# Performance work log

Hardware: AMD Instinct MI355X
Metric: run time of the kernel (lower is better)

The kernel has to match this reference:

```python
import jax, jax.numpy as jnp
import numpy as np

B = 8; C = 128; EXP = 4; H = 112; W = 112; K = 3; PAD = 1; STRIDE = 1
IN_C = C * EXP  # 512
EPS = 1e-5


def setup_inputs() -> dict:
    key = jax.random.key(0)
    ks = jax.random.split(key, 24)
    f32 = jnp.float32

    def n(k, shape, s=0.05):
        return jax.random.normal(k, shape, f32) * s

    def bn_params(k):
        k1, k2, k3, k4 = jax.random.split(k, 4)
        g = 1.0 + 0.1 * jax.random.normal(k1, (), f32)  # placeholder, per-channel below
        return k1, k2, k3, k4

    inp = {}
    inp["x"] = jax.random.normal(ks[0], (B, IN_C, H, W), f32)
    # conv1: 1x1, 512 -> 128
    inp["w1"] = n(ks[1], (C, IN_C))
    inp["b1"] = n(ks[2], (C,))
    # bn1
    inp["g1"] = 1.0 + 0.1 * jax.random.normal(ks[3], (C,), f32)
    inp["be1"] = 0.1 * jax.random.normal(ks[4], (C,), f32)
    inp["m1"] = 0.1 * jax.random.normal(ks[5], (C,), f32)
    inp["v1"] = 1.0 + 0.1 * jax.random.uniform(ks[6], (C,), f32)
    # offset conv: 3x3, C -> 18 (small weights so sampling offsets stay modest)
    inp["woff"] = n(ks[7], (2 * K * K, C, K, K), 0.01)
    inp["boff"] = jnp.zeros((2 * K * K,), f32)
    # deformable conv weight: 3x3, C -> C
    inp["wd"] = n(ks[8], (C, C, K, K))
    inp["bd"] = n(ks[9], (C,))
    # bn2
    inp["g2"] = 1.0 + 0.1 * jax.random.normal(ks[10], (C,), f32)
    inp["be2"] = 0.1 * jax.random.normal(ks[11], (C,), f32)
    inp["m2"] = 0.1 * jax.random.normal(ks[12], (C,), f32)
    inp["v2"] = 1.0 + 0.1 * jax.random.uniform(ks[13], (C,), f32)
    # conv2: 1x1, 128 -> 512
    inp["w2"] = n(ks[14], (IN_C, C))
    inp["b2"] = n(ks[15], (IN_C,))
    # bn3
    inp["g3"] = 1.0 + 0.1 * jax.random.normal(ks[16], (IN_C,), f32)
    inp["be3"] = 0.1 * jax.random.normal(ks[17], (IN_C,), f32)
    inp["m3"] = 0.1 * jax.random.normal(ks[18], (IN_C,), f32)
    inp["v3"] = 1.0 + 0.1 * jax.random.uniform(ks[19], (IN_C,), f32)
    return inp


def conv1x1(x, w, b):
    return jnp.einsum("oc,bchw->bohw", w, x) + b[None, :, None, None]


def bn(x, g, be, m, v):
    inv = g / jnp.sqrt(v + EPS)
    return x * inv[None, :, None, None] + (be - m * inv)[None, :, None, None]


def conv3x3(x, w, b):
    out = jax.lax.conv_general_dilated(
        x, w, (STRIDE, STRIDE), ((PAD, PAD), (PAD, PAD)),
        dimension_numbers=("NCHW", "OIHW", "NCHW"))
    return out + b[None, :, None, None]


def deform_conv(x, offset, w, b):
    # x: [B, Cin, H, W]; offset: [B, 2*K*K, Ho, Wo] (y,x interleaved per kernel pt)
    Bn, Cin, Hh, Ww = x.shape
    Ho, Wo = offset.shape[2], offset.shape[3]
    P = Ho * Wo
    off = offset.reshape(Bn, K * K, 2, Ho, Wo)
    kk = jnp.arange(K * K)
    ky = (kk // K).astype(jnp.float32)  # 0..2
    kx = (kk % K).astype(jnp.float32)
    base_y = jnp.arange(Ho, dtype=jnp.float32) * STRIDE - PAD
    base_x = jnp.arange(Wo, dtype=jnp.float32) * STRIDE - PAD
    py = base_y[None, None, :, None] + ky[None, :, None, None] + off[:, :, 0]  # [B,9,Ho,Wo]
    px = base_x[None, None, None, :] + kx[None, :, None, None] + off[:, :, 1]
    y0 = jnp.floor(py); x0 = jnp.floor(px)
    dy = (py - y0).reshape(Bn, 1, -1)  # [B,1,9*P]
    dx = (px - x0).reshape(Bn, 1, -1)
    x_flat = x.reshape(Bn, Cin, Hh * Ww)

    def gather(yi, xi):
        valid = ((yi >= 0) & (yi <= Hh - 1) & (xi >= 0) & (xi <= Ww - 1))
        yc = jnp.clip(yi, 0, Hh - 1).astype(jnp.int32)
        xc = jnp.clip(xi, 0, Ww - 1).astype(jnp.int32)
        idx = (yc * Ww + xc).reshape(Bn, -1)  # [B, 9*P]
        g = jax.vmap(lambda xb, ib: xb[:, ib])(x_flat, idx)  # [B, Cin, 9*P]
        return g * valid.reshape(Bn, 1, -1).astype(x.dtype)

    v00 = gather(y0, x0)
    v01 = gather(y0, x0 + 1)
    v10 = gather(y0 + 1, x0)
    v11 = gather(y0 + 1, x0 + 1)
    cols = (v00 * (1 - dy) * (1 - dx) + v01 * (1 - dy) * dx
            + v10 * dy * (1 - dx) + v11 * dy * dx)  # [B, Cin, 9*P]
    cols = cols.reshape(Bn, Cin * K * K, P)
    out = jnp.einsum("oi,bip->bop", w.reshape(w.shape[0], -1), cols)
    out = out + b[None, :, None]
    return out.reshape(Bn, w.shape[0], Ho, Wo)


def reference(x, w1, b1, g1, be1, m1, v1, woff, boff, wd, bd,
              g2, be2, m2, v2, w2, b2, g3, be3, m3, v3):
    out = jax.nn.relu(bn(conv1x1(x, w1, b1), g1, be1, m1, v1))
    offset = conv3x3(out, woff, boff)
    out = deform_conv(out, offset, wd, bd)
    out = bn(out, g2, be2, m2, v2)
    out = bn(conv1x1(out, w2, b2), g3, be3, m3, v3)
    return jax.nn.relu(out + x)
```

## Files before the change

### kernel.cpp

```cpp
#include <hip/hip_runtime.h>
#include <hip/hip_bf16.h>


typedef __attribute__((ext_vector_type(8))) short short8;
typedef __attribute__((ext_vector_type(4))) float f32x4;

constexpr int Bn = 8;
constexpr int IC = 512;
constexpr int Cc = 128;
constexpr int Hh = 112;
constexpr int Ww = 112;
constexpr int Pp = Hh * Ww;
constexpr float EPSf = 1e-5f;

constexpr size_t OFS_OFFS  = 0;
constexpr size_t OFS_OUT2B = 2097152;
constexpr size_t OFS_W1B   = (size_t)Bn * Pp * IC / 2;
constexpr size_t OFS_W2B   = OFS_W1B + (size_t)Cc * IC / 2;
constexpr size_t OFS_WDB   = OFS_W2B + (size_t)IC * Cc / 2;
constexpr size_t OFS_WOFB  = OFS_WDB + (size_t)9 * Cc * Cc / 2;

__device__ __forceinline__ ushort f2bf(float f) {
  uint u = __float_as_uint(f);
  return (ushort)((u + 0x7fffu + ((u >> 16) & 1u)) >> 16);
}
__device__ __forceinline__ float bfLO(uint u) {
  return __uint_as_float(u << 16);
}
__device__ __forceinline__ float bfHI(uint u) {
  return __uint_as_float(u & 0xffff0000u);
}
__device__ __forceinline__ uint cvtpk(float a, float b) {
  __hip_bfloat162 h = __float22bfloat162_rn(make_float2(a, b));
  return *(uint*)&h;
}

__global__ __launch_bounds__(256) void prep_kernel(
    const float* __restrict__ w1, const float* __restrict__ w2,
    const float* __restrict__ wd, const float* __restrict__ woff,
    float* __restrict__ ws) {
  ushort* w1b  = (ushort*)(ws + OFS_W1B);
  ushort* w2b  = (ushort*)(ws + OFS_W2B);
  ushort* wdb  = (ushort*)(ws + OFS_WDB);
  ushort* wofb = (ushort*)(ws + OFS_WOFB);
  const int n1 = Cc * IC;
  const int n2 = IC * Cc;
  const int n3 = 9 * Cc * Cc;
  const int n4 = 9 * 32 * Cc;
  const int total = n1 + n2 + n3 + n4;
  for (int idx = blockIdx.x * blockDim.x + threadIdx.x; idx < total;
       idx += gridDim.x * blockDim.x) {
    if (idx < n1) {
      w1b[idx] = f2bf(w1[idx]);
    } else if (idx < n1 + n2) {
      int t = idx - n1;
      w2b[t] = f2bf(w2[t]);
    } else if (idx < n1 + n2 + n3) {
      int t = idx - n1 - n2;
      int k = t / (Cc * Cc), r = t % (Cc * Cc);
      int oc = r / Cc, ic = r % Cc;
      wdb[t] = f2bf(wd[(oc * Cc + ic) * 9 + k]);
    } else {
      int t = idx - n1 - n2 - n3;
      int k = t / (32 * Cc), r = t % (32 * Cc);
      int oc = r / Cc, ic = r % Cc;
      wofb[t] = (oc < 18) ? f2bf(woff[(oc * Cc + ic) * 9 + k]) : (ushort)0;
    }
  }
}

__global__ __launch_bounds__(256) void k1_fused_mfma(
    const float* __restrict__ x, const ushort* __restrict__ w1b,
    const float* __restrict__ b1, const float* __restrict__ g1,
    const float* __restrict__ be1, const float* __restrict__ m1,
    const float* __restrict__ v1, ushort* __restrict__ out1b) {
  __shared__ ushort smem[26624];

  const int tid = threadIdx.x;
  const int lane = tid & 63;
  const int wv = tid >> 6;
  const int lr = lane & 15, lg = lane >> 4;
  const int orig = blockIdx.x;
  const int bid = (orig & 7) * 98 + (orig >> 3);
  const int bi = bid / 98;
  const int pblk = (bid % 98) * 128;

  float xs[2][4][2][2];
  short8 wsv[2][2];

#define BAR_LGKM asm volatile("s_waitcnt lgkmcnt(0)\ns_barrier" ::: "memory")

#define LOADX(c, s)                                                       \
  {                                                                       \
    const float* xb_ = x + ((size_t)bi * IC + (size_t)((c) * 32 + wv * 8)) * Pp \
                         + pblk + lane;                                   \
    _Pragma("unroll") for (int q = 0; q < 4; ++q) {                       \
      _Pragma("unroll") for (int p = 0; p < 2; ++p) {                     \
        xs[s][q][p][0] = xb_[(size_t)(2 * q + p) * Pp];                   \
        xs[s][q][p][1] = xb_[(size_t)(2 * q + p) * Pp + 64];              \
      }                                                                   \
    }                                                                     \
  }

#define LOADW(c, s)                                                       \
  {                                                                       \
    const ushort* wb_ = w1b + (size_t)(wv * 32 + (lane >> 2)) * IC        \
                            + (c) * 32 + (lane & 3) * 8;                  \
    wsv[s][0] = *(const short8*)(wb_);                                    \
    wsv[s][1] = *(const short8*)(wb_ + (size_t)16 * IC);                  \
  }

#define WRITE(c, s)                                                       \
  {                                                                       \
    char* atb_ = (char*)smem + ((c) & 1) * 16384;                         \
    _Pragma("unroll") for (int e = 0; e < 2; ++e) {                       \
      const int px_ = lane + 64 * e;                                      \
      uint4 pk_;                                                          \
      uint* pp_ = (uint*)&pk_;                                            \
      _Pragma("unroll") for (int q = 0; q < 4; ++q)                       \
        pp_[q] = cvtpk(xs[s][q][0][e], xs[s][q][1][e]);                   \
      *(uint4*)(atb_ + px_ * 128 + ((wv ^ (px_ & 7)) << 4)) = pk_;        \
    }                                                                     \
    ushort* wlb_ = smem + 16384 + ((c) & 1) * 5120;                       \
    *(short8*)(wlb_ + (wv * 32 + (lane >> 2)) * 40 + (lane & 3) * 8) = wsv[s][0]; \
    *(short8*)(wlb_ + (wv * 32 + 16 + (lane >> 2)) * 40 + (lane & 3) * 8) = wsv[s][1]; \
  }

  f32x4 acc[2][8];
#pragma unroll
  for (int m = 0; m < 2; ++m)
#pragma unroll
    for (int n = 0; n < 8; ++n) acc[m][n] = (f32x4)0.f;

  LOADX(0, 0) LOADW(0, 0)
  LOADX(1, 1) LOADW(1, 1)

#pragma unroll
  for (int c = 0; c < 16; ++c) {
    WRITE(c, c & 1);
    BAR_LGKM;
    if (c + 2 < 16) { LOADX(c + 2, c & 1) LOADW(c + 2, c & 1) }

    {
      const char* atb = (const char*)smem + (c & 1) * 16384;
      const ushort* wlb = smem + 16384 + (c & 1) * 5120;
      const int sw = (lg ^ (lr & 7)) << 4;
      short8 a0 = *(const short8*)(atb + (wv * 32 + lr) * 128 + sw);
      short8 a1 = *(const short8*)(atb + (wv * 32 + 16 + lr) * 128 + sw);
#pragma unroll
      for (int n = 0; n < 8; ++n) {
        short8 b = *(const short8*)(wlb + (n * 16 + lr) * 40 + lg * 8);
        acc[0][n] = __builtin_amdgcn_mfma_f32_16x16x32_bf16(a0, b, acc[0][n], 0, 0, 0);
        acc[1][n] = __builtin_amdgcn_mfma_f32_16x16x32_bf16(a1, b, acc[1][n], 0, 0, 0);
      }
    }
  }

#undef LOADX
#undef LOADW
#undef WRITE
#undef BAR_LGKM

  __syncthreads();

  ushort(*Ab)[136] = (ushort(*)[136])smem;
#pragma unroll
  for (int n = 0; n < 8; ++n) {
    int oc = n * 16 + lr;
    float inv = g1[oc] * rsqrtf(v1[oc] + EPSf);
    float sh = (b1[oc] - m1[oc]) * inv + be1[oc];
#pragma unroll
    for (int m = 0; m < 2; ++m) {
#pragma unroll
      for (int r = 0; r < 4; ++r) {
        int pl = wv * 32 + m * 16 + lg * 4 + r;
        Ab[pl][oc] = f2bf(fmaxf(acc[m][n][r] * inv + sh, 0.f));
      }
    }
  }
#pragma unroll
  for (int j = 0; j < 8; ++j) {
    int pl = wv * 32 + j * 4 + (lane >> 4);
    uint4 v = *(const uint4*)&Ab[pl][(lane & 15) * 8];
    *(uint4*)(out1b + ((size_t)bi * Pp + pblk + pl) * Cc + (lane & 15) * 8) = v;
  }
}

__global__ __launch_bounds__(256) void k3_deform_mfma(
    const ushort* __restrict__ out1b, const ushort* __restrict__ wofb,
    const float* __restrict__ boff,
    const ushort* __restrict__ wdb, const float* __restrict__ bd,
    const float* __restrict__ g2, const float* __restrict__ be2,
    const float* __restrict__ m2, const float* __restrict__ v2,
    ushort* __restrict__ out2b) {
  __shared__ ushort colsA[2][64][136];
  __shared__ float meta[9 * 64 * 8];

  const int tid = threadIdx.x;
  const int lane = tid & 63;
  const int wv = tid >> 6;
  const int lr = lane & 15, lg = lane >> 4;
  const int orig = blockIdx.x;
  const int bid = (orig & 7) * 196 + (orig >> 3);
  const int bi = bid / 196;
  const int p0 = (bid % 196) * 64;

  const ushort* src = out1b + (size_t)bi * Pp * Cc;
  float* pacc = (float*)colsA;

  {
    int ohm[4], owm[4];
#pragma unroll
    for (int m = 0; m < 4; ++m) {
      int p = p0 + m * 16 + lr;
      ohm[m] = p / Ww;
      owm[m] = p - ohm[m] * Ww;
    }
    f32x4 aco[4][2];
#pragma unroll
    for (int m = 0; m < 4; ++m) { aco[m][0] = (f32x4)0.f; aco[m][1] = (f32x4)0.f; }

    for (int k = wv; k < 9; k += 4) {
      const int kdy = k / 3 - 1, kdx = k % 3 - 1;
      const ushort* rp[4];
      bool val[4];
#pragma unroll
      for (int m = 0; m < 4; ++m) {
        int yy = ohm[m] + kdy, xx = owm[m] + kdx;
        val[m] = ((unsigned)yy < (unsigned)Hh) && ((unsigned)xx < (unsigned)Ww);
        int yc = min(max(yy, 0), Hh - 1), xc = min(max(xx, 0), Ww - 1);
        rp[m] = src + (size_t)(yc * Ww + xc) * Cc;
      }
#pragma unroll
      for (int ks = 0; ks < 4; ++ks) {
        short8 b0 = *(const short8*)(wofb + (size_t)(k * 32 + lr) * Cc + ks * 32 + 8 * lg);
        short8 b1v = *(const short8*)(wofb + (size_t)(k * 32 + 16 + lr) * Cc + ks * 32 + 8 * lg);
#pragma unroll
        for (int m = 0; m < 4; ++m) {
          short8 av = *(const short8*)(rp[m] + ks * 32 + 8 * lg);
          short8 a = val[m] ? av : (short8)0;
          aco[m][0] = __builtin_amdgcn_mfma_f32_16x16x32_bf16(a, b0, aco[m][0], 0, 0, 0);
          aco[m][1] = __builtin_amdgcn_mfma_f32_16x16x32_bf16(a, b1v, aco[m][1], 0, 0, 0);
        }
      }
    }
#pragma unroll
    for (int n = 0; n < 2; ++n)
#pragma unroll
      for (int m = 0; m < 4; ++m)
#pragma unroll
        for (int r = 0; r < 4; ++r) {
          int px = m * 16 + lg * 4 + r;
          pacc[(wv * 64 + px) * 33 + n * 16 + lr] = aco[m][n][r];
        }
  }
  __syncthreads();

  {
    const int p = p0 + lane;
    const int oh = p / Ww, ow = p - oh * Ww;
    for (int k = wv; k < 9; k += 4) {
      const int kdy = k / 3 - 1, kdx = k % 3 - 1;
      float offy = boff[2 * k], offx = boff[2 * k + 1];
#pragma unroll
      for (int w = 0; w < 4; ++w) {
        offy += pacc[(w * 64 + lane) * 33 + 2 * k];
        offx += pacc[(w * 64 + lane) * 33 + 2 * k + 1];
      }
      float py = (float)(oh + kdy) + offy;
      float pxf = (float)(ow + kdx) + offx;
      float y0f = floorf(py), x0f = floorf(pxf);
      float dy = py - y0f, dx = pxf - x0f;
      int y0 = (int)y0f, x0 = (int)x0f;
      int y1 = y0 + 1, x1 = x0 + 1;
      float wy0 = (y0 >= 0 && y0 < Hh) ? 1.f - dy : 0.f;
      float wy1 = (y1 >= 0 && y1 < Hh) ? dy : 0.f;
      float wx0 = (x0 >= 0 && x0 < Ww) ? 1.f - dx : 0.f;
      float wx1 = (x1 >= 0 && x1 < Ww) ? dx : 0.f;
      int yc0 = min(max(y0, 0), Hh - 1), yc1 = min(max(y1, 0), Hh - 1);
      int xc0 = min(max(x0, 0), Ww - 1), xc1 = min(max(x1, 0), Ww - 1);
      float* mp = &meta[(k * 64 + lane) * 8];
      mp[0] = wy0 * wx0;
      mp[1] = wy0 * wx1;
      mp[2] = wy1 * wx0;
      mp[3] = wy1 * wx1;
      int* ip = (int*)(mp + 4);
      ip[0] = (yc0 * Ww + xc0) * (Cc * 2);
      ip[1] = (yc0 * Ww + xc1) * (Cc * 2);
      ip[2] = (yc1 * Ww + xc0) * (Cc * 2);
      ip[3] = (yc1 * Ww + xc1) * (Cc * 2);
    }
  }
  __syncthreads();

  f32x4 acc[4][2];
#pragma unroll
  for (int m = 0; m < 4; ++m) { acc[m][0] = (f32x4)0.f; acc[m][1] = (f32x4)0.f; }

  const int pxq = lane >> 4;
  const int l16 = lane & 15;
  const char* sb = (const char*)src + l16 * 16;

  uint4 gv[4][4];
  float4 gw[4];

#define BAR_LGKM asm volatile("s_waitcnt lgkmcnt(0)\ns_barrier" ::: "memory")

#define ISSUE(kk, t)                                                     \
  {                                                                      \
    const int px_ = wv * 16 + (t) * 4 + pxq;                             \
    const float* mp_ = &meta[((kk) * 64 + px_) * 8];                     \
    gw[t] = *(const float4*)mp_;                                         \
    int4 o4_ = *(const int4*)(mp_ + 4);                                  \
    gv[t][0] = *(const uint4*)(sb + o4_.x);                              \
    gv[t][1] = *(const uint4*)(sb + o4_.y);                              \
    gv[t][2] = *(const uint4*)(sb + o4_.z);                              \
    gv[t][3] = *(const uint4*)(sb + o4_.w);                              \
  }

#define COMMIT(buf, t)                                                   \
  {                                                                      \
    const int px_ = wv * 16 + (t) * 4 + pxq;                             \
    float4 w4_ = gw[t];                                                  \
    uint4 pk_;                                                           \
    uint* pkp_ = (uint*)&pk_;                                            \
    _Pragma("unroll")                                                    \
    for (int j = 0; j < 4; ++j) {                                        \
      uint a0_ = ((const uint*)&gv[t][0])[j];                            \
      uint a1_ = ((const uint*)&gv[t][1])[j];                            \
      uint a2_ = ((const uint*)&gv[t][2])[j];                            \
      uint a3_ = ((const uint*)&gv[t][3])[j];                            \
      float lo_ = w4_.x * bfLO(a0_) + w4_.y * bfLO(a1_)                  \
                + w4_.z * bfLO(a2_) + w4_.w * bfLO(a3_);                 \
      float hi_ = w4_.x * bfHI(a0_) + w4_.y * bfHI(a1_)                  \
                + w4_.z * bfHI(a2_) + w4_.w * bfHI(a3_);                 \
      pkp_[j] = cvtpk(lo_, hi_);                                         \
    }                                                                    \
    *(uint4*)&colsA[buf][px_][l16 * 8] = pk_;                            \
  }

  ISSUE(0, 0) ISSUE(0, 1) ISSUE(0, 2) ISSUE(0, 3)
  COMMIT(0, 0) COMMIT(0, 1) COMMIT(0, 2) COMMIT(0, 3)
  ISSUE(1, 0) ISSUE(1, 1) ISSUE(1, 2) ISSUE(1, 3)
  BAR_LGKM;

  for (int k = 0; k < 9; ++k) {
    const int cur = k & 1;
    const int nxt = cur ^ 1;
    const ushort* wk = wdb + (size_t)k * Cc * Cc + (size_t)(wv * 32) * Cc;

#pragma unroll
    for (int ks = 0; ks < 4; ++ks) {
      short8 b0 = *(const short8*)(wk + lr * Cc + ks * 32 + 8 * lg);
      short8 b1v = *(const short8*)(wk + (16 + lr) * Cc + ks * 32 + 8 * lg);
#pragma unroll
      for (int m = 0; m < 4; ++m) {
        short8 a = *(const short8*)&colsA[cur][m * 16 + lr][ks * 32 + 8 * lg];
        acc[m][0] = __builtin_amdgcn_mfma_f32_16x16x32_bf16(a, b0, acc[m][0], 0, 0, 0);
        acc[m][1] = __builtin_amdgcn_mfma_f32_16x16x32_bf16(a, b1v, acc[m][1], 0, 0, 0);
      }
    }

    if (k < 8) {
      COMMIT(nxt, 0)
      if (k < 7) { ISSUE(k + 2, 0) }
      COMMIT(nxt, 1)
      if (k < 7) { ISSUE(k + 2, 1) }
      COMMIT(nxt, 2)
      if (k < 7) { ISSUE(k + 2, 2) }
      COMMIT(nxt, 3)
      if (k < 7) { ISSUE(k + 2, 3) }
      BAR_LGKM;
    }
  }

#undef ISSUE
#undef COMMIT
#undef BAR_LGKM

#pragma unroll
  for (int n = 0; n < 2; ++n) {
    int oc = wv * 32 + n * 16 + lr;
    float inv = g2[oc] * rsqrtf(v2[oc] + EPSf);
    float sh = (bd[oc] - m2[oc]) * inv + be2[oc];
#pragma unroll
    for (int m = 0; m < 4; ++m) {
#pragma unroll
      for (int r = 0; r < 4; ++r) {
        int p = p0 + m * 16 + lg * 4 + r;
        out2b[((size_t)bi * Pp + p) * Cc + oc] = f2bf(acc[m][n][r] * inv + sh);
      }
    }
  }
}

__global__ __launch_bounds__(256, 2) void k4_mfma(
    const ushort* __restrict__ out2b, const ushort* __restrict__ w2b,
    const float* __restrict__ b2, const float* __restrict__ g3,
    const float* __restrict__ be3, const float* __restrict__ m3,
    const float* __restrict__ v3, const float* __restrict__ x,
    float* __restrict__ out) {
  __shared__ float obuf[2][16][260];

  const int tid = threadIdx.x;
  const int lane = tid & 63;
  const int wv = tid >> 6;
  const int lr = lane & 15, lg = lane >> 4;
  const int orig = blockIdx.x;
  const int bid = (orig & 7) * 392 + (orig >> 3);
  const int bi = bid / 392;
  const int r392 = bid % 392;
  const int oc_t = r392 / 49;
  const int pblk = (r392 % 49) * 256;
  const int p0 = pblk + wv * 64;
  const int ocb = oc_t * 64;

  const ushort* A = out2b + ((size_t)bi * Pp + p0) * Cc;
  const ushort* Bw = w2b + (size_t)ocb * Cc;

  float4 xv[4][4];
#pragma unroll
  for (int n = 0; n < 4; ++n)
#pragma unroll
    for (int it = 0; it < 4; ++it) {
      int oc = ocb + n * 16 + it * 4 + wv;
      xv[n][it] = *(const float4*)(x + ((size_t)bi * IC + oc) * Pp + pblk + lane * 4);
    }

  f32x4 acc[4][4];
#pragma unroll
  for (int m = 0; m < 4; ++m)
#pragma unroll
    for (int n = 0; n < 4; ++n) acc[m][n] = (f32x4)0.f;

#pragma unroll
  for (int ks = 0; ks < 4; ++ks) {
    short8 a[4];
#pragma unroll
    for (int m = 0; m < 4; ++m)
      a[m] = *(const short8*)(A + (size_t)(m * 16 + lr) * Cc + ks * 32 + 8 * lg);
#pragma unroll
    for (int n = 0; n < 4; ++n) {
      short8 b = *(const short8*)(Bw + (size_t)(n * 16 + lr) * Cc + ks * 32 + 8 * lg);
#pragma unroll
      for (int m = 0; m < 4; ++m)
        acc[m][n] = __builtin_amdgcn_mfma_f32_16x16x32_bf16(a[m], b, acc[m][n], 0, 0, 0);
    }
  }

#pragma unroll
  for (int n = 0; n < 4; ++n) {
    {
      int ocw = ocb + n * 16 + lr;
      float inv = g3[ocw] * rsqrtf(v3[ocw] + EPSf);
      float sh = (b2[ocw] - m3[ocw]) * inv + be3[ocw];
      float(*buf)[260] = obuf[n & 1];
#pragma unroll
      for (int m = 0; m < 4; ++m) {
        float4 o;
        o.x = acc[m][n][0] * inv + sh;
        o.y = acc[m][n][1] * inv + sh;
        o.z = acc[m][n][2] * inv + sh;
        o.w = acc[m][n][3] * inv + sh;
        *(float4*)&buf[lr][wv * 64 + m * 16 + lg * 4] = o;
      }
    }
    __syncthreads();
    {
      const float(*buf)[260] = obuf[n & 1];
#pragma unroll
      for (int it = 0; it < 4; ++it) {
        int r = it * 4 + wv;
        int oc = ocb + n * 16 + r;
        float4 v = *(const float4*)&buf[r][lane * 4];
        float4 xr = xv[n][it];
        float4 o;
        o.x = fmaxf(v.x + xr.x, 0.f);
        o.y = fmaxf(v.y + xr.y, 0.f);
        o.z = fmaxf(v.z + xr.z, 0.f);
        o.w = fmaxf(v.w + xr.w, 0.f);
        *(float4*)(out + ((size_t)bi * IC + oc) * Pp + pblk + lane * 4) = o;
      }
    }
  }
}

extern "C" void kernel_launch(void* const* d_in, const int* in_sizes, int n_in,
                              void* d_out, int out_size, void* d_ws, size_t ws_size,
                              hipStream_t stream) {
  const float* x    = (const float*)d_in[0];
  const float* w1   = (const float*)d_in[1];
  const float* b1   = (const float*)d_in[2];
  const float* g1   = (const float*)d_in[3];
  const float* be1  = (const float*)d_in[4];
  const float* m1   = (const float*)d_in[5];
  const float* v1   = (const float*)d_in[6];
  const float* woff = (const float*)d_in[7];
  const float* boff = (const float*)d_in[8];
  const float* wd   = (const float*)d_in[9];
  const float* bd   = (const float*)d_in[10];
  const float* g2   = (const float*)d_in[11];
  const float* be2  = (const float*)d_in[12];
  const float* m2   = (const float*)d_in[13];
  const float* v2   = (const float*)d_in[14];
  const float* w2   = (const float*)d_in[15];
  const float* b2   = (const float*)d_in[16];
  const float* g3   = (const float*)d_in[17];
  const float* be3  = (const float*)d_in[18];
  const float* m3   = (const float*)d_in[19];
  const float* v3   = (const float*)d_in[20];

  float* ws   = (float*)d_ws;
  float* out  = (float*)d_out;
  ushort* out2b = (ushort*)(ws + OFS_OUT2B);
  ushort* w1b   = (ushort*)(ws + OFS_W1B);
  ushort* w2b   = (ushort*)(ws + OFS_W2B);
  ushort* wdb   = (ushort*)(ws + OFS_WDB);
  ushort* wofb  = (ushort*)(ws + OFS_WOFB);
  ushort* out1b = (ushort*)d_out;

  prep_kernel<<<512, 256, 0, stream>>>(w1, w2, wd, woff, ws);
  k1_fused_mfma<<<Bn * 98, 256, 0, stream>>>(x, w1b, b1, g1, be1, m1, v1, out1b);
  k3_deform_mfma<<<Bn * 196, 256, 0, stream>>>(out1b, wofb, boff, wdb, bd,
                                               g2, be2, m2, v2, out2b);
  k4_mfma<<<Bn * 392, 256, 0, stream>>>(out2b, w2b, b2, g3, be3, m3, v3, x, out);
}
```

Measured before the change: 311.5 us.

## Single-buffer deform cols tile and reuse meta smem for offset partials

Shrinks the deform kernel's shared memory by replacing the double-buffered colsA tile with a single buffer and storing only the 18 needed offset-conv partials in the meta array rather than colsA. Offsets are read into registers before a new barrier so that meta can be overwritten. The goal is lower LDS per block so more blocks can be resident per CU. The cost is an extra barrier per k-step, which serializes the bilinear commit with the MFMA reads and gives up overlap between the gather and the matrix math.

Measured after the change: 315.3 us. About the same (+1.2%).

```diff
diff --git a/kernel.cpp b/kernel.cpp
--- a/kernel.cpp
+++ b/kernel.cpp
@@ -13,7 +13,6 @@
 constexpr int Pp = Hh * Ww;
 constexpr float EPSf = 1e-5f;
 
-constexpr size_t OFS_OFFS  = 0;
 constexpr size_t OFS_OUT2B = 2097152;
 constexpr size_t OFS_W1B   = (size_t)Bn * Pp * IC / 2;
 constexpr size_t OFS_W2B   = OFS_W1B + (size_t)Cc * IC / 2;
@@ -193,7 +192,7 @@
     const float* __restrict__ g2, const float* __restrict__ be2,
     const float* __restrict__ m2, const float* __restrict__ v2,
     ushort* __restrict__ out2b) {
-  __shared__ ushort colsA[2][64][136];
+  __shared__ ushort colsA[64][136];
   __shared__ float meta[9 * 64 * 8];
 
   const int tid = threadIdx.x;
@@ -206,7 +205,7 @@
   const int p0 = (bid % 196) * 64;
 
   const ushort* src = out1b + (size_t)bi * Pp * Cc;
-  float* pacc = (float*)colsA;
+  float* pacc = meta;
 
   {
     int ohm[4], owm[4];
@@ -245,50 +244,64 @@
       }
     }
 #pragma unroll
-    for (int n = 0; n < 2; ++n)
-#pragma unroll
-      for (int m = 0; m < 4; ++m)
-#pragma unroll
-        for (int r = 0; r < 4; ++r) {
-          int px = m * 16 + lg * 4 + r;
-          pacc[(wv * 64 + px) * 33 + n * 16 + lr] = aco[m][n][r];
-        }
+    for (int m = 0; m < 4; ++m)
+#pragma unroll
+      for (int r = 0; r < 4; ++r) {
+        int px = m * 16 + lg * 4 + r;
+        pacc[(wv * 64 + px) * 18 + lr] = aco[m][0][r];
+        if (lr < 2)
+          pacc[(wv * 64 + px) * 18 + 16 + lr] = aco[m][1][r];
+      }
   }
   __syncthreads();
 
   {
     const int p = p0 + lane;
     const int oh = p / Ww, ow = p - oh * Ww;
-    for (int k = wv; k < 9; k += 4) {
-      const int kdy = k / 3 - 1, kdx = k % 3 - 1;
-      float offy = boff[2 * k], offx = boff[2 * k + 1];
-#pragma unroll
-      for (int w = 0; w < 4; ++w) {
-        offy += pacc[(w * 64 + lane) * 33 + 2 * k];
-        offx += pacc[(w * 64 + lane) * 33 + 2 * k + 1];
-      }
-      float py = (float)(oh + kdy) + offy;
-      float pxf = (float)(ow + kdx) + offx;
-      float y0f = floorf(py), x0f = floorf(pxf);
-      float dy = py - y0f, dx = pxf - x0f;
-      int y0 = (int)y0f, x0 = (int)x0f;
-      int y1 = y0 + 1, x1 = x0 + 1;
-      float wy0 = (y0 >= 0 && y0 < Hh) ? 1.f - dy : 0.f;
-      float wy1 = (y1 >= 0 && y1 < Hh) ? dy : 0.f;
-      float wx0 = (x0 >= 0 && x0 < Ww) ? 1.f - dx : 0.f;
-      float wx1 = (x1 >= 0 && x1 < Ww) ? dx : 0.f;
-      int yc0 = min(max(y0, 0), Hh - 1), yc1 = min(max(y1, 0), Hh - 1);
-      int xc0 = min(max(x0, 0), Ww - 1), xc1 = min(max(x1, 0), Ww - 1);
-      float* mp = &meta[(k * 64 + lane) * 8];
-      mp[0] = wy0 * wx0;
-      mp[1] = wy0 * wx1;
-      mp[2] = wy1 * wx0;
-      mp[3] = wy1 * wx1;
-      int* ip = (int*)(mp + 4);
-      ip[0] = (yc0 * Ww + xc0) * (Cc * 2);
-      ip[1] = (yc0 * Ww + xc1) * (Cc * 2);
-      ip[2] = (yc1 * Ww + xc0) * (Cc * 2);
-      ip[3] = (yc1 * Ww + xc1) * (Cc * 2);
+    float offy[3], offx[3];
+#pragma unroll
+    for (int j = 0; j < 3; ++j) {
+      const int k = wv + 4 * j;
+      if (k < 9) {
+        float oy = boff[2 * k], ox = boff[2 * k + 1];
+#pragma unroll
+        for (int w = 0; w < 4; ++w) {
+          oy += pacc[(w * 64 + lane) * 18 + 2 * k];
+          ox += pacc[(w * 64 + lane) * 18 + 2 * k + 1];
+        }
+        offy[j] = oy;
+        offx[j] = ox;
+      }
+    }
+    __syncthreads();
+#pragma unroll
+    for (int j = 0; j < 3; ++j) {
+      const int k = wv + 4 * j;
+      if (k < 9) {
+        const int kdy = k / 3 - 1, kdx = k % 3 - 1;
+        float py = (float)(oh + kdy) + offy[j];
+        float pxf = (float)(ow + kdx) + offx[j];
+        float y0f = floorf(py), x0f = floorf(pxf);
+        float dy = py - y0f, dx = pxf - x0f;
+        int y0 = (int)y0f, x0 = (int)x0f;
+        int y1 = y0 + 1, x1 = x0 + 1;
+        float wy0 = (y0 >= 0 && y0 < Hh) ? 1.f - dy : 0.f;
+        float wy1 = (y1 >= 0 && y1 < Hh) ? dy : 0.f;
+        float wx0 = (x0 >= 0 && x0 < Ww) ? 1.f - dx : 0.f;
+        float wx1 = (x1 >= 0 && x1 < Ww) ? dx : 0.f;
+        int yc0 = min(max(y0, 0), Hh - 1), yc1 = min(max(y1, 0), Hh - 1);
+        int xc0 = min(max(x0, 0), Ww - 1), xc1 = min(max(x1, 0), Ww - 1);
+        float* mp = &meta[(k * 64 + lane) * 8];
+        mp[0] = wy0 * wx0;
+        mp[1] = wy0 * wx1;
+        mp[2] = wy1 * wx0;
+        mp[3] = wy1 * wx1;
+        int* ip = (int*)(mp + 4);
+        ip[0] = (yc0 * Ww + xc0) * (Cc * 2);
+        ip[1] = (yc0 * Ww + xc1) * (Cc * 2);
+        ip[2] = (yc1 * Ww + xc0) * (Cc * 2);
+        ip[3] = (yc1 * Ww + xc1) * (Cc * 2);
+      }
     }
   }
   __syncthreads();
@@ -318,7 +331,7 @@
     gv[t][3] = *(const uint4*)(sb + o4_.w);                              \
   }
 
-#define COMMIT(buf, t)                                                   \
+#define COMMIT(t)                                                        \
   {                                                                      \
     const int px_ = wv * 16 + (t) * 4 + pxq;                             \
     float4 w4_ = gw[t];                                                  \
@@ -336,17 +349,15 @@
                 + w4_.z * bfHI(a2_) + w4_.w * bfHI(a3_);                 \
       pkp_[j] = cvtpk(lo_, hi_);                                         \
     }                                                                    \
-    *(uint4*)&colsA[buf][px_][l16 * 8] = pk_;                            \
+    *(uint4*)&colsA[px_][l16 * 8] = pk_;                                 \
   }
 
   ISSUE(0, 0) ISSUE(0, 1) ISSUE(0, 2) ISSUE(0, 3)
-  COMMIT(0, 0) COMMIT(0, 1) COMMIT(0, 2) COMMIT(0, 3)
+  COMMIT(0) COMMIT(1) COMMIT(2) COMMIT(3)
   ISSUE(1, 0) ISSUE(1, 1) ISSUE(1, 2) ISSUE(1, 3)
   BAR_LGKM;
 
   for (int k = 0; k < 9; ++k) {
-    const int cur = k & 1;
-    const int nxt = cur ^ 1;
     const ushort* wk = wdb + (size_t)k * Cc * Cc + (size_t)(wv * 32) * Cc;
 
 #pragma unroll
@@ -355,20 +366,21 @@
       short8 b1v = *(const short8*)(wk + (16 + lr) * Cc + ks * 32 + 8 * lg);
 #pragma unroll
       for (int m = 0; m < 4; ++m) {
-        short8 a = *(const short8*)&colsA[cur][m * 16 + lr][ks * 32 + 8 * lg];
+        short8 a = *(const short8*)&colsA[m * 16 + lr][ks * 32 + 8 * lg];
         acc[m][0] = __builtin_amdgcn_mfma_f32_16x16x32_bf16(a, b0, acc[m][0], 0, 0, 0);
         acc[m][1] = __builtin_amdgcn_mfma_f32_16x16x32_bf16(a, b1v, acc[m][1], 0, 0, 0);
       }
     }
 
     if (k < 8) {
-      COMMIT(nxt, 0)
+      BAR_LGKM;
+      COMMIT(0)
       if (k < 7) { ISSUE(k + 2, 0) }
-      COMMIT(nxt, 1)
+      COMMIT(1)
       if (k < 7) { ISSUE(k + 2, 1) }
-      COMMIT(nxt, 2)
+      COMMIT(2)
       if (k < 7) { ISSUE(k + 2, 2) }
-      COMMIT(nxt, 3)
+      COMMIT(3)
       if (k < 7) { ISSUE(k + 2, 3) }
       BAR_LGKM;
     }
```
